# Performance work log

Hardware: AMD Instinct MI355X
Metric: run time of the kernel (lower is better)

Reference implementation:

```python
import jax, jax.numpy as jnp
import numpy as np

HIDDEN = 1024
NUM_HEADS = 16
HEAD_DIM = HIDDEN // NUM_HEADS
PROJ = 1024
B, T = 32, 2048


def setup_inputs() -> dict:
    key = jax.random.key(0)
    k1, k2, k3, k4 = jax.random.split(key, 4)
    hidden_states = jax.random.normal(k1, (B, T, HIDDEN), dtype=jnp.float32)
    mask = jnp.ones((B, T), dtype=jnp.int32)
    # torch Linear: y = x @ W.T + b; store transposed weights [in, out]
    kv_w = jax.random.normal(k2, (HIDDEN, 2 * HIDDEN), dtype=jnp.float32) * 0.02
    kv_b = jnp.zeros((2 * HIDDEN,), dtype=jnp.float32)
    out_w = jax.random.normal(k3, (HIDDEN, PROJ), dtype=jnp.float32) * 0.02
    out_b = jnp.zeros((PROJ,), dtype=jnp.float32)
    query = jax.random.normal(k4, (HIDDEN,), dtype=jnp.float32) * 0.02
    return {
        "hidden_states": hidden_states,
        "mask": mask,
        "kv_w": kv_w,
        "kv_b": kv_b,
        "out_w": out_w,
        "out_b": out_b,
        "query": query,
    }


def reference(hidden_states, mask, kv_w, kv_b, out_w, out_b, query):
    b = hidden_states.shape[0]
    kv = hidden_states @ kv_w + kv_b                      # [B, T, 2H]
    k, v = jnp.split(kv, 2, axis=-1)                      # [B, T, H] each
    q = query.reshape(NUM_HEADS, HEAD_DIM)                # [h, d]
    k = k.reshape(b, -1, NUM_HEADS, HEAD_DIM)             # [B, T, h, d]
    v = v.reshape(b, -1, NUM_HEADS, HEAD_DIM)
    scale = 1.0 / HEAD_DIM ** 0.5
    attn = jnp.einsum('hd,bjhd->bhj', q * scale, k)       # [B, h, T]
    attn = jnp.where(mask[:, None, :] == 0, -jnp.inf, attn)
    attn = jax.nn.softmax(attn, axis=-1)
    out = jnp.einsum('bhj,bjhd->bhd', attn, v)            # [B, h, d]
    out = out.reshape(b, -1)                              # [B, H]
    return out @ out_w + out_b                            # [B, PROJ]
```

## Files before the change

### kernel.cpp

```cpp
#include <hip/hip_runtime.h>
#include <hip/hip_bf16.h>
#include <math.h>


#define NH 16

__global__ __launch_bounds__(256) void k_wqk(const float* __restrict__ q,
                                             const float* __restrict__ kvw,
                                             float* __restrict__ wqk) {
  int t = blockIdx.x * 256 + threadIdx.x;
  int c = t >> 4, h = t & 15;
  const float4* kvw4 = (const float4*)kvw;
  const float4* q4 = (const float4*)q;
  int wb = c * 512 + h * 16;
  int qb = h * 16;
  float acc = 0.f;
#pragma unroll
  for (int i = 0; i < 16; ++i) {
    float4 w = kvw4[wb + i];
    float4 qq = q4[qb + i];
    acc += w.x * qq.x + w.y * qq.y + w.z * qq.z + w.w * qq.w;
  }
  wqk[h * 1024 + c] = acc * 0.125f;
}

__global__ __launch_bounds__(256) void k_logits(const float* __restrict__ hid,
                                                const float* __restrict__ wqk_g,
                                                float* __restrict__ logits) {
  __shared__ float4 lwqk[16][256];
  int tid = threadIdx.x;
  int b = blockIdx.y, jt = blockIdx.x;
  const float4* wq4 = (const float4*)wqk_g;
  for (int i = tid; i < 4096; i += 256) {
    int h = i >> 8, c4 = i & 255;
    lwqk[h][(c4 + h) & 255] = wq4[i];
  }
  __syncthreads();
  int lane = tid & 63, wid = tid >> 6;
  int jr = lane >> 4, h = lane & 15;
  const float4* hid4 = (const float4*)hid;
  for (int rg = 0; rg < 8; ++rg) {
    int j = jt * 128 + rg * 16 + wid * 4 + jr;
    int base = (b * 2048 + j) * 256;
    float a0 = 0.f, a1 = 0.f, a2 = 0.f, a3 = 0.f;
    for (int c4 = 0; c4 < 256; c4 += 4) {
      float4 x0 = hid4[base + c4 + 0];
      float4 x1 = hid4[base + c4 + 1];
      float4 x2 = hid4[base + c4 + 2];
      float4 x3 = hid4[base + c4 + 3];
      float4 w0 = lwqk[h][(c4 + 0 + h) & 255];
      float4 w1 = lwqk[h][(c4 + 1 + h) & 255];
      float4 w2 = lwqk[h][(c4 + 2 + h) & 255];
      float4 w3 = lwqk[h][(c4 + 3 + h) & 255];
      a0 += x0.x * w0.x + x0.y * w0.y + x0.z * w0.z + x0.w * w0.w;
      a1 += x1.x * w1.x + x1.y * w1.y + x1.z * w1.z + x1.w * w1.w;
      a2 += x2.x * w2.x + x2.y * w2.y + x2.z * w2.z + x2.w * w2.w;
      a3 += x3.x * w3.x + x3.y * w3.y + x3.z * w3.z + x3.w * w3.w;
    }
    logits[(b * NH + h) * 2048 + j] = (a0 + a1) + (a2 + a3);
  }
}

__global__ __launch_bounds__(256) void k_softmax(float* __restrict__ lg,
                                                 const int* __restrict__ mask) {
  int bh = blockIdx.x;
  int b = bh >> 4;
  int tid = threadIdx.x;
  __shared__ float redm[4];
  __shared__ float reds[4];
  float4* lg4 = (float4*)lg + bh * 512;
  const int4* m4 = (const int4*)mask + b * 512;
  float4 la = lg4[tid], lb = lg4[tid + 256];
  int4 ma = m4[tid], mb = m4[tid + 256];
  const float NI = -INFINITY;
  la.x = ma.x ? la.x : NI; la.y = ma.y ? la.y : NI;
  la.z = ma.z ? la.z : NI; la.w = ma.w ? la.w : NI;
  lb.x = mb.x ? lb.x : NI; lb.y = mb.y ? lb.y : NI;
  lb.z = mb.z ? lb.z : NI; lb.w = mb.w ? lb.w : NI;
  float mx = fmaxf(fmaxf(fmaxf(la.x, la.y), fmaxf(la.z, la.w)),
                   fmaxf(fmaxf(lb.x, lb.y), fmaxf(lb.z, lb.w)));
  for (int off = 32; off; off >>= 1) mx = fmaxf(mx, __shfl_xor(mx, off));
  if ((tid & 63) == 0) redm[tid >> 6] = mx;
  __syncthreads();
  mx = fmaxf(fmaxf(redm[0], redm[1]), fmaxf(redm[2], redm[3]));
  la.x = expf(la.x - mx); la.y = expf(la.y - mx);
  la.z = expf(la.z - mx); la.w = expf(la.w - mx);
  lb.x = expf(lb.x - mx); lb.y = expf(lb.y - mx);
  lb.z = expf(lb.z - mx); lb.w = expf(lb.w - mx);
  float s = la.x + la.y + la.z + la.w + lb.x + lb.y + lb.z + lb.w;
  for (int off = 32; off; off >>= 1) s += __shfl_xor(s, off);
  if ((tid & 63) == 0) reds[tid >> 6] = s;
  __syncthreads();
  s = reds[0] + reds[1] + reds[2] + reds[3];
  float inv = 1.0f / s;
  la.x *= inv; la.y *= inv; la.z *= inv; la.w *= inv;
  lb.x *= inv; lb.y *= inv; lb.z *= inv; lb.w *= inv;
  lg4[tid] = la;
  lg4[tid + 256] = lb;
}

#define FMA4(A, S) { A.x = fmaf(S, x.x, A.x); A.y = fmaf(S, x.y, A.y); \
                     A.z = fmaf(S, x.z, A.z); A.w = fmaf(S, x.w, A.w); }
__global__ __launch_bounds__(256) void k_pool(const float* __restrict__ hid,
                                              const float* __restrict__ w_g,
                                              float* __restrict__ pooled) {
  __shared__ float lw[256][16];
  int tid = threadIdx.x;
  int ch = blockIdx.x, b = blockIdx.y;
  int j0 = ch * 256;
  for (int i = tid; i < 4096; i += 256) {
    int jj = i >> 4, h = i & 15;
    lw[jj][h] = w_g[(b * NH + h) * 2048 + j0 + jj];
  }
  __syncthreads();
  float4 acc[16];
#pragma unroll
  for (int h = 0; h < 16; ++h) acc[h] = make_float4(0.f, 0.f, 0.f, 0.f);
  const float4* hid4 = (const float4*)hid + (b * 2048 + j0) * 256 + tid;
#pragma unroll 2
  for (int jj = 0; jj < 256; ++jj) {
    float4 x = hid4[jj * 256];
    float4 w0 = *(const float4*)&lw[jj][0];
    float4 w1 = *(const float4*)&lw[jj][4];
    float4 w2 = *(const float4*)&lw[jj][8];
    float4 w3 = *(const float4*)&lw[jj][12];
    FMA4(acc[0], w0.x) FMA4(acc[1], w0.y) FMA4(acc[2], w0.z) FMA4(acc[3], w0.w)
    FMA4(acc[4], w1.x) FMA4(acc[5], w1.y) FMA4(acc[6], w1.z) FMA4(acc[7], w1.w)
    FMA4(acc[8], w2.x) FMA4(acc[9], w2.y) FMA4(acc[10], w2.z) FMA4(acc[11], w2.w)
    FMA4(acc[12], w3.x) FMA4(acc[13], w3.y) FMA4(acc[14], w3.z) FMA4(acc[15], w3.w)
  }
  float* pbase = pooled + b * NH * 1024 + tid * 4;
#pragma unroll
  for (int h = 0; h < 16; ++h) {
    float* p = pbase + h * 1024;
    atomicAdd(p + 0, acc[h].x);
    atomicAdd(p + 1, acc[h].y);
    atomicAdd(p + 2, acc[h].z);
    atomicAdd(p + 3, acc[h].w);
  }
}

__global__ __launch_bounds__(256) void k_vproj(const float* __restrict__ pooled,
                                               const float* __restrict__ kvw,
                                               const float* __restrict__ kvb,
                                               float* __restrict__ out_pre) {
  int bh = blockIdx.x;
  int b = bh >> 4, h = bh & 15;
  int tid = threadIdx.x;
  __shared__ float pool[1024];
  __shared__ float red[4][64];
  const float4* p4 = (const float4*)pooled + (b * NH + h) * 256 + tid;
  *(float4*)&pool[tid * 4] = p4[0];
  __syncthreads();
  int cq = tid >> 6, lane = tid & 63;
  int coff = lane >> 4, d4 = lane & 15;
  const float4* kv4 = (const float4*)kvw;
  float4 a = make_float4(0.f, 0.f, 0.f, 0.f);
#pragma unroll 4
  for (int i = 0; i < 64; ++i) {
    int c = cq * 256 + i * 4 + coff;
    float pc = pool[c];
    float4 wv = kv4[c * 512 + 256 + h * 16 + d4];
    a.x = fmaf(pc, wv.x, a.x); a.y = fmaf(pc, wv.y, a.y);
    a.z = fmaf(pc, wv.z, a.z); a.w = fmaf(pc, wv.w, a.w);
  }
  a.x += __shfl_xor(a.x, 16); a.y += __shfl_xor(a.y, 16);
  a.z += __shfl_xor(a.z, 16); a.w += __shfl_xor(a.w, 16);
  a.x += __shfl_xor(a.x, 32); a.y += __shfl_xor(a.y, 32);
  a.z += __shfl_xor(a.z, 32); a.w += __shfl_xor(a.w, 32);
  if (coff == 0) *(float4*)&red[cq][d4 * 4] = a;
  __syncthreads();
  if (tid < 64) {
    float o = red[0][tid] + red[1][tid] + red[2][tid] + red[3][tid]
            + kvb[1024 + h * 64 + tid];
    out_pre[b * 1024 + h * 64 + tid] = o;
  }
}

__global__ __launch_bounds__(256) void k_final(const float* __restrict__ out_pre,
                                               const float* __restrict__ ow,
                                               const float* __restrict__ ob,
                                               float* __restrict__ out) {
  int pc = blockIdx.x, b = blockIdx.y;
  int p = pc * 256 + threadIdx.x;
  float acc = ob[p];
  const float* xp = out_pre + b * 1024;
#pragma unroll 8
  for (int k = 0; k < 1024; ++k) {
    acc = fmaf(xp[k], ow[k * 1024 + p], acc);
  }
  out[b * 1024 + p] = acc;
}

extern "C" void kernel_launch(void* const* d_in, const int* in_sizes, int n_in,
                              void* d_out, int out_size, void* d_ws, size_t ws_size,
                              hipStream_t stream) {
  const float* hid = (const float*)d_in[0];
  const int* mask = (const int*)d_in[1];
  const float* kvw = (const float*)d_in[2];
  const float* kvb = (const float*)d_in[3];
  const float* ow  = (const float*)d_in[4];
  const float* ob  = (const float*)d_in[5];
  const float* q   = (const float*)d_in[6];
  float* ws = (float*)d_ws;
  float* wqk     = ws;
  float* logits  = ws + 16384;
  float* pooled  = ws + 16384 + 1048576;
  float* out_pre = pooled + 524288;

  hipMemsetAsync(pooled, 0, 524288 * sizeof(float), stream);
  hipLaunchKernelGGL(k_wqk,     dim3(64),      dim3(256), 0, stream, q, kvw, wqk);
  hipLaunchKernelGGL(k_logits,  dim3(16, 32),  dim3(256), 0, stream, hid, wqk, logits);
  hipLaunchKernelGGL(k_softmax, dim3(512),     dim3(256), 0, stream, logits, mask);
  hipLaunchKernelGGL(k_pool,    dim3(8, 32),   dim3(256), 0, stream, hid, logits, pooled);
  hipLaunchKernelGGL(k_vproj,   dim3(512),     dim3(256), 0, stream, pooled, kvw, kvb, out_pre);
  hipLaunchKernelGGL(k_final,   dim3(4, 32),   dim3(256), 0, stream, out_pre, ow, ob, (float*)d_out);
}
```

Baseline: 698.1 us.

## Widen logits/pool blocks and replace pool atomics with per-chunk partial sums

k_logits now runs 512 threads per block with half as many row iterations, and k_pool runs 1024 threads where each wave handles 4 heads over a 64-float4 column segment, so each thread holds 16 accumulators instead of 64. When the workspace is large enough, k_pool writes per-chunk partials that k_vproj sums, replacing the memset and global atomics. This raises occupancy and removes atomic contention. In exchange hidden_states is read four times per pool block (once per head-group wave), relying on cache hits, and partials cost extra workspace traffic.

```diff
diff --git a/kernel.cpp b/kernel.cpp
--- a/kernel.cpp
+++ b/kernel.cpp
@@ -24,14 +24,14 @@
   wqk[h * 1024 + c] = acc * 0.125f;
 }
 
-__global__ __launch_bounds__(256) void k_logits(const float* __restrict__ hid,
-                                                const float* __restrict__ wqk_g,
-                                                float* __restrict__ logits) {
+__global__ __launch_bounds__(512, 4) void k_logits(const float* __restrict__ hid,
+                                                   const float* __restrict__ wqk_g,
+                                                   float* __restrict__ logits) {
   __shared__ float4 lwqk[16][256];
   int tid = threadIdx.x;
   int b = blockIdx.y, jt = blockIdx.x;
   const float4* wq4 = (const float4*)wqk_g;
-  for (int i = tid; i < 4096; i += 256) {
+  for (int i = tid; i < 4096; i += 512) {
     int h = i >> 8, c4 = i & 255;
     lwqk[h][(c4 + h) & 255] = wq4[i];
   }
@@ -39,8 +39,8 @@
   int lane = tid & 63, wid = tid >> 6;
   int jr = lane >> 4, h = lane & 15;
   const float4* hid4 = (const float4*)hid;
-  for (int rg = 0; rg < 8; ++rg) {
-    int j = jt * 128 + rg * 16 + wid * 4 + jr;
+  for (int rg = 0; rg < 4; ++rg) {
+    int j = jt * 128 + rg * 32 + wid * 4 + jr;
     int base = (b * 2048 + j) * 256;
     float a0 = 0.f, a1 = 0.f, a2 = 0.f, a3 = 0.f;
     for (int c4 = 0; c4 < 256; c4 += 4) {
@@ -99,58 +99,81 @@
   lg4[tid + 256] = lb;
 }
 
-#define FMA4(A, S) { A.x = fmaf(S, x.x, A.x); A.y = fmaf(S, x.y, A.y); \
-                     A.z = fmaf(S, x.z, A.z); A.w = fmaf(S, x.w, A.w); }
-__global__ __launch_bounds__(256) void k_pool(const float* __restrict__ hid,
-                                              const float* __restrict__ w_g,
-                                              float* __restrict__ pooled) {
+__global__ __launch_bounds__(1024, 4) void k_pool(const float* __restrict__ hid,
+                                                  const float* __restrict__ w_g,
+                                                  float* __restrict__ dst,
+                                                  int use_part) {
   __shared__ float lw[256][16];
   int tid = threadIdx.x;
   int ch = blockIdx.x, b = blockIdx.y;
   int j0 = ch * 256;
-  for (int i = tid; i < 4096; i += 256) {
+  for (int i = tid; i < 4096; i += 1024) {
     int jj = i >> 4, h = i & 15;
     lw[jj][h] = w_g[(b * NH + h) * 2048 + j0 + jj];
   }
   __syncthreads();
-  float4 acc[16];
-#pragma unroll
-  for (int h = 0; h < 16; ++h) acc[h] = make_float4(0.f, 0.f, 0.f, 0.f);
-  const float4* hid4 = (const float4*)hid + (b * 2048 + j0) * 256 + tid;
-#pragma unroll 2
+  int lane = tid & 63, wave = tid >> 6;
+  int hg = wave >> 2, cseg = wave & 3;
+  int h0 = hg * 4;
+  int f = cseg * 64 + lane;
+  const float4* hrow = (const float4*)hid + (b * 2048 + j0) * 256 + f;
+  float4 a0 = make_float4(0.f, 0.f, 0.f, 0.f);
+  float4 a1 = a0, a2 = a0, a3 = a0;
+#pragma unroll 4
   for (int jj = 0; jj < 256; ++jj) {
-    float4 x = hid4[jj * 256];
-    float4 w0 = *(const float4*)&lw[jj][0];
-    float4 w1 = *(const float4*)&lw[jj][4];
-    float4 w2 = *(const float4*)&lw[jj][8];
-    float4 w3 = *(const float4*)&lw[jj][12];
-    FMA4(acc[0], w0.x) FMA4(acc[1], w0.y) FMA4(acc[2], w0.z) FMA4(acc[3], w0.w)
-    FMA4(acc[4], w1.x) FMA4(acc[5], w1.y) FMA4(acc[6], w1.z) FMA4(acc[7], w1.w)
-    FMA4(acc[8], w2.x) FMA4(acc[9], w2.y) FMA4(acc[10], w2.z) FMA4(acc[11], w2.w)
-    FMA4(acc[12], w3.x) FMA4(acc[13], w3.y) FMA4(acc[14], w3.z) FMA4(acc[15], w3.w)
-  }
-  float* pbase = pooled + b * NH * 1024 + tid * 4;
-#pragma unroll
-  for (int h = 0; h < 16; ++h) {
-    float* p = pbase + h * 1024;
-    atomicAdd(p + 0, acc[h].x);
-    atomicAdd(p + 1, acc[h].y);
-    atomicAdd(p + 2, acc[h].z);
-    atomicAdd(p + 3, acc[h].w);
-  }
-}
-
-__global__ __launch_bounds__(256) void k_vproj(const float* __restrict__ pooled,
+    float4 x = hrow[jj * 256];
+    float w0 = lw[jj][h0 + 0];
+    float w1 = lw[jj][h0 + 1];
+    float w2 = lw[jj][h0 + 2];
+    float w3 = lw[jj][h0 + 3];
+    a0.x = fmaf(w0, x.x, a0.x); a0.y = fmaf(w0, x.y, a0.y);
+    a0.z = fmaf(w0, x.z, a0.z); a0.w = fmaf(w0, x.w, a0.w);
+    a1.x = fmaf(w1, x.x, a1.x); a1.y = fmaf(w1, x.y, a1.y);
+    a1.z = fmaf(w1, x.z, a1.z); a1.w = fmaf(w1, x.w, a1.w);
+    a2.x = fmaf(w2, x.x, a2.x); a2.y = fmaf(w2, x.y, a2.y);
+    a2.z = fmaf(w2, x.z, a2.z); a2.w = fmaf(w2, x.w, a2.w);
+    a3.x = fmaf(w3, x.x, a3.x); a3.y = fmaf(w3, x.y, a3.y);
+    a3.z = fmaf(w3, x.z, a3.z); a3.w = fmaf(w3, x.w, a3.w);
+  }
+  if (use_part) {
+    float4* p4 = (float4*)dst + ch * 131072 + (b * NH + h0) * 256 + f;
+    p4[0 * 256] = a0;
+    p4[1 * 256] = a1;
+    p4[2 * 256] = a2;
+    p4[3 * 256] = a3;
+  } else {
+    float* p = dst + (b * NH + h0) * 1024 + f * 4;
+    atomicAdd(p + 0,    a0.x); atomicAdd(p + 1,    a0.y);
+    atomicAdd(p + 2,    a0.z); atomicAdd(p + 3,    a0.w);
+    p += 1024;
+    atomicAdd(p + 0,    a1.x); atomicAdd(p + 1,    a1.y);
+    atomicAdd(p + 2,    a1.z); atomicAdd(p + 3,    a1.w);
+    p += 1024;
+    atomicAdd(p + 0,    a2.x); atomicAdd(p + 1,    a2.y);
+    atomicAdd(p + 2,    a2.z); atomicAdd(p + 3,    a2.w);
+    p += 1024;
+    atomicAdd(p + 0,    a3.x); atomicAdd(p + 1,    a3.y);
+    atomicAdd(p + 2,    a3.z); atomicAdd(p + 3,    a3.w);
+  }
+}
+
+__global__ __launch_bounds__(256) void k_vproj(const float* __restrict__ src,
                                                const float* __restrict__ kvw,
                                                const float* __restrict__ kvb,
-                                               float* __restrict__ out_pre) {
+                                               float* __restrict__ out_pre,
+                                               int nch) {
   int bh = blockIdx.x;
   int b = bh >> 4, h = bh & 15;
   int tid = threadIdx.x;
   __shared__ float pool[1024];
   __shared__ float red[4][64];
-  const float4* p4 = (const float4*)pooled + (b * NH + h) * 256 + tid;
-  *(float4*)&pool[tid * 4] = p4[0];
+  const float4* p4 = (const float4*)src + (b * NH + h) * 256 + tid;
+  float4 s = p4[0];
+  for (int ch = 1; ch < nch; ++ch) {
+    float4 v = p4[ch * 131072];
+    s.x += v.x; s.y += v.y; s.z += v.z; s.w += v.w;
+  }
+  *(float4*)&pool[tid * 4] = s;
   __syncthreads();
   int cq = tid >> 6, lane = tid & 63;
   int coff = lane >> 4, d4 = lane & 15;
@@ -203,16 +226,21 @@
   const float* ob  = (const float*)d_in[5];
   const float* q   = (const float*)d_in[6];
   float* ws = (float*)d_ws;
-  float* wqk     = ws;
-  float* logits  = ws + 16384;
-  float* pooled  = ws + 16384 + 1048576;
-  float* out_pre = pooled + 524288;
-
-  hipMemsetAsync(pooled, 0, 524288 * sizeof(float), stream);
-  hipLaunchKernelGGL(k_wqk,     dim3(64),      dim3(256), 0, stream, q, kvw, wqk);
-  hipLaunchKernelGGL(k_logits,  dim3(16, 32),  dim3(256), 0, stream, hid, wqk, logits);
-  hipLaunchKernelGGL(k_softmax, dim3(512),     dim3(256), 0, stream, logits, mask);
-  hipLaunchKernelGGL(k_pool,    dim3(8, 32),   dim3(256), 0, stream, hid, logits, pooled);
-  hipLaunchKernelGGL(k_vproj,   dim3(512),     dim3(256), 0, stream, pooled, kvw, kvb, out_pre);
-  hipLaunchKernelGGL(k_final,   dim3(4, 32),   dim3(256), 0, stream, out_pre, ow, ob, (float*)d_out);
-}
+  float* wqk    = ws;
+  float* logits = ws + 16384;
+  float* buf    = ws + 16384 + 1048576;
+
+  const int use_part = (ws_size >= (size_t)21168128) ? 1 : 0;
+  float* out_pre = buf + (use_part ? 4194304 : 524288);
+  const int nch = use_part ? 8 : 1;
+
+  if (!use_part) {
+    hipMemsetAsync(buf, 0, 524288 * sizeof(float), stream);
+  }
+  hipLaunchKernelGGL(k_wqk,     dim3(64),      dim3(256),  0, stream, q, kvw, wqk);
+  hipLaunchKernelGGL(k_logits,  dim3(16, 32),  dim3(512),  0, stream, hid, wqk, logits);
+  hipLaunchKernelGGL(k_softmax, dim3(512),     dim3(256),  0, stream, logits, mask);
+  hipLaunchKernelGGL(k_pool,    dim3(8, 32),   dim3(1024), 0, stream, hid, logits, buf, use_part);
+  hipLaunchKernelGGL(k_vproj,   dim3(512),     dim3(256),  0, stream, buf, kvw, kvb, out_pre, nch);
+  hipLaunchKernelGGL(k_final,   dim3(4, 32),   dim3(256),  0, stream, out_pre, ow, ob, (float*)d_out);
+}
```

Result: faster. 631.2 us (-9.6%).
